# Optimization experiments

Measured on AMD Instinct MI355X. Metric: run time of the kernel, lower is better.

## Reference

```python
import jax, jax.numpy as jnp
import numpy as np

D_MODEL = 1024
N_HEADS = 16
D_KV = 64
B, S = 2, 2048


def setup_inputs() -> dict:
    key = jax.random.key(0)
    ks = jax.random.split(key, 7)
    scale = 1.0 / np.sqrt(D_MODEL)
    return {
        "query": jax.random.normal(ks[0], (B, S, D_MODEL), jnp.float32),
        "key": jax.random.normal(ks[1], (B, S, D_MODEL), jnp.float32),
        "value": jax.random.normal(ks[2], (B, S, D_MODEL), jnp.float32),
        "mask": jnp.zeros((B, 1, 1, S), jnp.float32),
        "Wq": jax.random.normal(ks[3], (D_MODEL, N_HEADS * D_KV), jnp.float32) * scale,
        "Wk": jax.random.normal(ks[4], (D_MODEL, N_HEADS * D_KV), jnp.float32) * scale,
        "Wv": jax.random.normal(ks[5], (D_MODEL, N_HEADS * D_KV), jnp.float32) * scale,
        "Wo": jax.random.normal(ks[6], (N_HEADS * D_KV, D_MODEL), jnp.float32) * scale,
    }


def _split_heads(x):
    b, s, _ = x.shape
    return x.reshape(b, s, N_HEADS, D_KV).transpose(0, 2, 1, 3)  # [B,H,S,Dk]


def reference(query, key, value, mask, Wq, Wk, Wv, Wo):
    q = _split_heads(query @ Wq)
    k = _split_heads(key @ Wk)
    v = _split_heads(value @ Wv)
    scores = jnp.einsum("bhqd,bhkd->bhqk", q, k) / jnp.sqrt(
        jnp.asarray(D_KV, scores_dtype := q.dtype)
    )
    scores = scores + mask
    attn = jax.nn.softmax(scores, axis=-1)  # dropout_rate=0 -> identity
    ctx = jnp.einsum("bhqk,bhkd->bhqd", attn, v)
    ctx = ctx.transpose(0, 2, 1, 3).reshape(query.shape[0], -1, N_HEADS * D_KV)
    hidden = ctx @ Wo
    return hidden
```

## Files before the change

kernel.cpp:

```cpp
#include <hip/hip_runtime.h>
#include <hip/hip_bf16.h>
#include <stdint.h>

typedef __bf16 bf16;
typedef __bf16 bf16x8 __attribute__((ext_vector_type(8)));
typedef __bf16 bf16x4 __attribute__((ext_vector_type(4)));
typedef float  f32x4  __attribute__((ext_vector_type(4)));
typedef float  f32x16 __attribute__((ext_vector_type(16)));

#define S_LEN  2048
#define NH     16
#define DKV    64
#define DMODEL 1024
#define LOG2E  1.4426950408889634f

__device__ __forceinline__ void async_load16(const void* g, void* l) {
  __builtin_amdgcn_global_load_lds(
      (const __attribute__((address_space(1))) uint32_t*)(uintptr_t)g,
      (__attribute__((address_space(3))) uint32_t*)(uintptr_t)l,
      16, 0, 0);
}

__global__ void cast_qkv(const float* __restrict__ q, const float* __restrict__ k,
                         const float* __restrict__ v,
                         bf16* __restrict__ qo, bf16* __restrict__ ko, bf16* __restrict__ vo)
{
  int z = blockIdx.y;
  const float* in = (z == 0) ? q : (z == 1) ? k : v;
  bf16* out = (z == 0) ? qo : (z == 1) ? ko : vo;
  int i = blockIdx.x * 256 + threadIdx.x;
  const float4* in4 = (const float4*)in;
  float4 a = in4[2 * i];
  float4 c = in4[2 * i + 1];
  bf16x8 o;
  o[0] = (bf16)a.x; o[1] = (bf16)a.y; o[2] = (bf16)a.z; o[3] = (bf16)a.w;
  o[4] = (bf16)c.x; o[5] = (bf16)c.y; o[6] = (bf16)c.z; o[7] = (bf16)c.w;
  ((bf16x8*)out)[i] = o;
}

__global__ void transpose_w(const float* __restrict__ W0, const float* __restrict__ W1,
                            const float* __restrict__ W2, const float* __restrict__ W3,
                            bf16* __restrict__ T0, bf16* __restrict__ T1,
                            bf16* __restrict__ T2, bf16* __restrict__ T3)
{
  int z = blockIdx.z;
  const float* W = (z == 0) ? W0 : (z == 1) ? W1 : (z == 2) ? W2 : W3;
  bf16* T = (z == 0) ? T0 : (z == 1) ? T1 : (z == 2) ? T2 : T3;
  __shared__ float tile[32][33];
  int n0 = blockIdx.x * 32, k0 = blockIdx.y * 32;
  int tx = threadIdx.x, ty = threadIdx.y;
  for (int i = 0; i < 32; i += 8)
    tile[ty + i][tx] = W[(size_t)(k0 + ty + i) * DMODEL + n0 + tx];
  __syncthreads();
  for (int i = 0; i < 32; i += 8)
    T[(size_t)(n0 + ty + i) * DMODEL + k0 + tx] = (bf16)tile[tx][ty + i];
}

template<int TM, int MODE>
__global__ __launch_bounds__(256) void gemm_bt(
    const bf16* __restrict__ A0, const bf16* __restrict__ A1, const bf16* __restrict__ A2,
    const bf16* __restrict__ B0, const bf16* __restrict__ B1, const bf16* __restrict__ B2,
    void* __restrict__ C0, void* __restrict__ C1, void* __restrict__ C2,
    int M, int N, int K)
{
  constexpr int MI = TM / 32;
  __shared__ __align__(16) bf16 As[TM * 32];
  __shared__ __align__(16) bf16 Bs[128 * 32];
  int z = blockIdx.z;
  const bf16* A  = (z == 0) ? A0 : (z == 1) ? A1 : A2;
  const bf16* Bt = (z == 0) ? B0 : (z == 1) ? B1 : B2;
  void* C        = (z == 0) ? C0 : (z == 1) ? C1 : C2;

  const int m0 = blockIdx.y * TM;
  const int n0 = blockIdx.x * 128;
  const int tid = threadIdx.x;
  const int lane = tid & 63;
  const int wave = tid >> 6;
  const int wm = (wave >> 1) * (TM / 2);
  const int wn = (wave & 1) * 64;
  const int row = lane & 15;
  const int quad = lane >> 4;

  f32x4 acc[MI][4];
  for (int i = 0; i < MI; ++i)
    for (int j = 0; j < 4; ++j) acc[i][j] = (f32x4){0.f, 0.f, 0.f, 0.f};

  const int nk = K >> 5;
  for (int kt = 0; kt < nk; ++kt) {
    __syncthreads();
    const int kk = kt << 5;
    for (int j = 0; j < TM / 64; ++j) {
      int base = j * 256 + wave * 64;
      int idx = base + lane;
      int r = idx >> 2;
      int cb = (idx & 3) << 4;
      async_load16((const char*)(A + (size_t)(m0 + r) * K + kk) + cb,
                   (char*)As + (size_t)base * 16);
    }
    for (int j = 0; j < 2; ++j) {
      int base = j * 256 + wave * 64;
      int idx = base + lane;
      int r = idx >> 2;
      int cb = (idx & 3) << 4;
      async_load16((const char*)(Bt + (size_t)(n0 + r) * K + kk) + cb,
                   (char*)Bs + (size_t)base * 16);
    }
    __syncthreads();
    bf16x8 af[MI], bfr[4];
    for (int i = 0; i < MI; ++i)
      af[i] = *(const bf16x8*)(As + (wm + i * 16 + row) * 32 + quad * 8);
    for (int j = 0; j < 4; ++j)
      bfr[j] = *(const bf16x8*)(Bs + (wn + j * 16 + row) * 32 + quad * 8);
    for (int i = 0; i < MI; ++i)
      for (int j = 0; j < 4; ++j)
        acc[i][j] = __builtin_amdgcn_mfma_f32_16x16x32_bf16(af[i], bfr[j], acc[i][j], 0, 0, 0);
  }

  if (MODE == 0) {
    float* Cf = (float*)C;
    for (int i = 0; i < MI; ++i)
      for (int j = 0; j < 4; ++j)
        for (int r = 0; r < 4; ++r) {
          int gm = m0 + wm + i * 16 + quad * 4 + r;
          int gn = n0 + wn + j * 16 + row;
          Cf[(size_t)gm * N + gn] = acc[i][j][r];
        }
  } else if (z != 2) {
    bf16* Cb = (bf16*)C;
    for (int i = 0; i < MI; ++i)
      for (int j = 0; j < 4; ++j)
        for (int r = 0; r < 4; ++r) {
          int gm = m0 + wm + i * 16 + quad * 4 + r;
          int gn = n0 + wn + j * 16 + row;
          int b = gm >> 11, s = gm & 2047;
          int h = gn >> 6,  d = gn & 63;
          Cb[(((size_t)(b * NH + h)) * S_LEN + s) * DKV + d] = (bf16)acc[i][j][r];
        }
  } else {
    bf16* Cb = (bf16*)C;
    for (int i = 0; i < MI; ++i)
      for (int j = 0; j < 4; ++j) {
        int gm = m0 + wm + i * 16 + quad * 4;
        int gn = n0 + wn + j * 16 + row;
        int b = gm >> 11, s = gm & 2047;
        int h = gn >> 6,  d = gn & 63;
        bf16x4 t;
        for (int r = 0; r < 4; ++r) t[r] = (bf16)acc[i][j][r];
        *(bf16x4*)(Cb + (((size_t)(b * NH + h)) * DKV + d) * S_LEN + s) = t;
      }
  }
}

__global__ __launch_bounds__(256, 4) void attn_kernel(
    const bf16* __restrict__ Qh, const bf16* __restrict__ Kh, const bf16* __restrict__ Vth,
    const float* __restrict__ mask, bf16* __restrict__ ctx)
{
  __shared__ __align__(16) bf16 Ks[64 * 64];
  __shared__ __align__(16) bf16 Kext[64 * 16];
  __shared__ __align__(16) bf16 Vts[64 * 64];
  __shared__ __align__(16) float lsumS[4 * 32];

  const int bh = blockIdx.y;
  const int b = bh >> 4;
  const int h = bh & 15;
  const int q0 = blockIdx.x * 128;
  const int tid = threadIdx.x;
  const int lane = tid & 63;
  const int wave = tid >> 6;
  const int ln = lane & 31;
  const int hi = lane >> 5;
  const float SC2 = 0.125f * LOG2E;

  const int qg = q0 + wave * 32 + ln;
  bf16x8 qf[5];
  {
    const bf16* qrow = Qh + ((size_t)bh * S_LEN + qg) * DKV;
    for (int c = 0; c < 4; ++c)
      qf[c] = *(const bf16x8*)(qrow + c * 16 + hi * 8);
    bf16x8 z;
    for (int u = 0; u < 8; ++u) z[u] = (bf16)0.f;
    if (hi == 0) z[0] = (bf16)1.0f;
    qf[4] = z;
  }

  f32x16 O[2];
  for (int nb = 0; nb < 2; ++nb)
    for (int i = 0; i < 16; ++i) O[nb][i] = 0.f;
  float lsum = 0.f;

  for (int kv0 = 0; kv0 < S_LEN; kv0 += 64) {
    __syncthreads();
    for (int j = 0; j < 2; ++j) {
      int base = j * 256 + wave * 64;
      int idx = base + lane;
      int r = idx >> 3;
      int cc = (idx & 7) ^ (r & 7);
      async_load16(Kh + ((size_t)bh * S_LEN + kv0 + r) * DKV + cc * 8,
                   (char*)Ks + (size_t)base * 16);
      async_load16(Vth + ((size_t)bh * DKV + r) * S_LEN + kv0 + cc * 8,
                   (char*)Vts + (size_t)base * 16);
    }
    if (tid < 64) {
      float m8 = mask[b * S_LEN + kv0 + tid] * 8.0f;
      bf16x8 e0, zz;
      for (int u = 0; u < 8; ++u) { e0[u] = (bf16)0.f; zz[u] = (bf16)0.f; }
      e0[0] = (bf16)m8;
      *(bf16x8*)(Kext + tid * 16)     = e0;
      *(bf16x8*)(Kext + tid * 16 + 8) = zz;
    }
    __syncthreads();

    f32x16 Sm[2];
    for (int i = 0; i < 16; ++i) { Sm[0][i] = 0.f; Sm[1][i] = 0.f; }
    for (int c = 0; c < 5; ++c) {
      bf16x8 k0, k1;
      if (c < 4) {
        k0 = *(const bf16x8*)(Ks + (ln)      * 64 + (((2 * c + hi) ^ (ln & 7)) << 3));
        k1 = *(const bf16x8*)(Ks + (32 + ln) * 64 + (((2 * c + hi) ^ (ln & 7)) << 3));
      } else {
        k0 = *(const bf16x8*)(Kext + ln * 16 + hi * 8);
        k1 = *(const bf16x8*)(Kext + (32 + ln) * 16 + hi * 8);
      }
      Sm[0] = __builtin_amdgcn_mfma_f32_32x32x16_bf16(k0, qf[c], Sm[0], 0, 0, 0);
      Sm[1] = __builtin_amdgcn_mfma_f32_32x32x16_bf16(k1, qf[c], Sm[1], 0, 0, 0);
    }

    for (int cg = 0; cg < 4; ++cg) {
      int mb = cg >> 1, g = cg & 1;
      bf16x8 ap;
      float ls0 = 0.f;
      for (int u = 0; u < 8; ++u) {
        float p = __builtin_amdgcn_exp2f(Sm[mb][g * 8 + u] * SC2);
        ls0 += p;
        ap[u] = (bf16)p;
      }
      lsum += ls0;
      for (int nb = 0; nb < 2; ++nb) {
        int d = nb * 32 + ln;
        int ch0 = ((2 * g + 4 * mb))     ^ (d & 7);
        int ch1 = ((1 + 2 * g + 4 * mb)) ^ (d & 7);
        bf16x4 lo = *(const bf16x4*)(Vts + d * 64 + ch0 * 8 + hi * 4);
        bf16x4 hv = *(const bf16x4*)(Vts + d * 64 + ch1 * 8 + hi * 4);
        bf16x8 bv;
        for (int u = 0; u < 4; ++u) { bv[u] = lo[u]; bv[u + 4] = hv[u]; }
        O[nb] = __builtin_amdgcn_mfma_f32_32x32x16_bf16(ap, bv, O[nb], 0, 0, 0);
      }
    }
  }

  float lt = lsum + __shfl_xor(lsum, 32, 64);
  if (lane < 32) lsumS[wave * 32 + lane] = 1.0f / lt;
  __builtin_amdgcn_s_waitcnt(0);

  for (int g = 0; g < 4; ++g) {
    f32x4 ri = *(const f32x4*)(lsumS + wave * 32 + g * 8 + hi * 4);
    for (int nb = 0; nb < 2; ++nb)
      for (int j = 0; j < 4; ++j) {
        int qrow = q0 + wave * 32 + j + 8 * g + 4 * hi;
        float v = O[nb][g * 4 + j] * ri[j];
        ctx[((size_t)b * S_LEN + qrow) * DMODEL + h * DKV + nb * 32 + ln] = (bf16)v;
      }
  }
}

extern "C" void kernel_launch(void* const* d_in, const int* in_sizes, int n_in,
                              void* d_out, int out_size, void* d_ws, size_t ws_size,
                              hipStream_t stream)
{
  const float* query = (const float*)d_in[0];
  const float* key_  = (const float*)d_in[1];
  const float* value = (const float*)d_in[2];
  const float* mask  = (const float*)d_in[3];
  const float* Wq = (const float*)d_in[4];
  const float* Wk = (const float*)d_in[5];
  const float* Wv = (const float*)d_in[6];
  const float* Wo = (const float*)d_in[7];

  char* ws = (char*)d_ws;
  const size_t MB = (size_t)1 << 20;
  bf16* qb  = (bf16*)(ws + 0 * MB);
  bf16* kb  = (bf16*)(ws + 8 * MB);
  bf16* vb  = (bf16*)(ws + 16 * MB);
  bf16* wqt = (bf16*)(ws + 24 * MB);
  bf16* wkt = (bf16*)(ws + 26 * MB);
  bf16* wvt = (bf16*)(ws + 28 * MB);
  bf16* wot = (bf16*)(ws + 30 * MB);
  bf16* qh  = (bf16*)(ws + 32 * MB);
  bf16* kh  = (bf16*)(ws + 40 * MB);
  bf16* vth = (bf16*)(ws + 48 * MB);
  bf16* ctx = (bf16*)(ws + 0 * MB);

  cast_qkv<<<dim3(2048, 3), 256, 0, stream>>>(query, key_, value, qb, kb, vb);
  transpose_w<<<dim3(32, 32, 4), dim3(32, 8), 0, stream>>>(Wq, Wk, Wv, Wo, wqt, wkt, wvt, wot);
  gemm_bt<128, 1><<<dim3(8, 32, 3), 256, 0, stream>>>(qb, kb, vb, wqt, wkt, wvt,
                                                      (void*)qh, (void*)kh, (void*)vth,
                                                      4096, 1024, 1024);
  attn_kernel<<<dim3(16, 32), 256, 0, stream>>>(qh, kh, vth, mask, ctx);
  gemm_bt<64, 0><<<dim3(8, 64, 1), 256, 0, stream>>>(ctx, ctx, ctx, wot, wot, wot,
                                                     d_out, d_out, d_out,
                                                     4096, 1024, 1024);
}
```

Baseline: 251.5 us.

## Split attention over two KV halves, add combine kernel, pre-permute V tiles

The attention kernel now splits the key/value sequence into two halves along a new grid dimension, writing unnormalized fp32 partial outputs and row sums, and a new combine kernel sums them, normalizes and writes bf16 context. The V projection epilogue writes V in a tile-permuted layout, so each 64x64 tile loads contiguously and reads no longer need XOR swizzle. The mask is added in fp32 before exp2 instead of through an extra MFMA step. This doubles the attention grid to fill more CUs, at the cost of an extra launch and fp32 partial-result traffic. Softmax still skips max subtraction, so the split needs no rescaling.

```diff
diff --git a/kernel.cpp b/kernel.cpp
--- a/kernel.cpp
+++ b/kernel.cpp
@@ -144,26 +144,27 @@
         int gn = n0 + wn + j * 16 + row;
         int b = gm >> 11, s = gm & 2047;
         int h = gn >> 6,  d = gn & 63;
+        int bh = b * NH + h;
+        int tile = s >> 6, kb = (s & 63) >> 2;
         bf16x4 t;
         for (int r = 0; r < 4; ++r) t[r] = (bf16)acc[i][j][r];
-        *(bf16x4*)(Cb + (((size_t)(b * NH + h)) * DKV + d) * S_LEN + s) = t;
+        *(bf16x4*)(Cb + ((((size_t)bh * 32 + tile) * 16 + kb) * 64 + d) * 4) = t;
       }
   }
 }
 
 __global__ __launch_bounds__(256, 4) void attn_kernel(
-    const bf16* __restrict__ Qh, const bf16* __restrict__ Kh, const bf16* __restrict__ Vth,
-    const float* __restrict__ mask, bf16* __restrict__ ctx)
+    const bf16* __restrict__ Qh, const bf16* __restrict__ Kh, const bf16* __restrict__ Vperm,
+    const float* __restrict__ mask, float* __restrict__ Opart, float* __restrict__ Lpart)
 {
   __shared__ __align__(16) bf16 Ks[64 * 64];
-  __shared__ __align__(16) bf16 Kext[64 * 16];
   __shared__ __align__(16) bf16 Vts[64 * 64];
-  __shared__ __align__(16) float lsumS[4 * 32];
+  __shared__ __align__(16) float masks2[64];
 
   const int bh = blockIdx.y;
   const int b = bh >> 4;
-  const int h = bh & 15;
   const int q0 = blockIdx.x * 128;
+  const int zh = blockIdx.z;
   const int tid = threadIdx.x;
   const int lane = tid & 63;
   const int wave = tid >> 6;
@@ -172,15 +173,11 @@
   const float SC2 = 0.125f * LOG2E;
 
   const int qg = q0 + wave * 32 + ln;
-  bf16x8 qf[5];
+  bf16x8 qf[4];
   {
     const bf16* qrow = Qh + ((size_t)bh * S_LEN + qg) * DKV;
     for (int c = 0; c < 4; ++c)
       qf[c] = *(const bf16x8*)(qrow + c * 16 + hi * 8);
-    bf16x8 z;
-    for (int u = 0; u < 8; ++u) z[u] = (bf16)0.f;
-    if (hi == 0) z[0] = (bf16)1.0f;
-    qf[4] = z;
   }
 
   f32x16 O[2];
@@ -188,8 +185,10 @@
     for (int i = 0; i < 16; ++i) O[nb][i] = 0.f;
   float lsum = 0.f;
 
-  for (int kv0 = 0; kv0 < S_LEN; kv0 += 64) {
+  for (int it = 0; it < 16; ++it) {
+    const int kv0 = zh * 1024 + it * 64;
     __syncthreads();
+    const bf16* vtile = Vperm + ((size_t)bh * 32 + (kv0 >> 6)) * (64 * 64);
     for (int j = 0; j < 2; ++j) {
       int base = j * 256 + wave * 64;
       int idx = base + lane;
@@ -197,50 +196,42 @@
       int cc = (idx & 7) ^ (r & 7);
       async_load16(Kh + ((size_t)bh * S_LEN + kv0 + r) * DKV + cc * 8,
                    (char*)Ks + (size_t)base * 16);
-      async_load16(Vth + ((size_t)bh * DKV + r) * S_LEN + kv0 + cc * 8,
+      async_load16(vtile + (size_t)idx * 8,
                    (char*)Vts + (size_t)base * 16);
     }
-    if (tid < 64) {
-      float m8 = mask[b * S_LEN + kv0 + tid] * 8.0f;
-      bf16x8 e0, zz;
-      for (int u = 0; u < 8; ++u) { e0[u] = (bf16)0.f; zz[u] = (bf16)0.f; }
-      e0[0] = (bf16)m8;
-      *(bf16x8*)(Kext + tid * 16)     = e0;
-      *(bf16x8*)(Kext + tid * 16 + 8) = zz;
-    }
+    if (tid < 64) masks2[tid] = mask[b * S_LEN + kv0 + tid] * LOG2E;
     __syncthreads();
 
     f32x16 Sm[2];
     for (int i = 0; i < 16; ++i) { Sm[0][i] = 0.f; Sm[1][i] = 0.f; }
-    for (int c = 0; c < 5; ++c) {
-      bf16x8 k0, k1;
-      if (c < 4) {
-        k0 = *(const bf16x8*)(Ks + (ln)      * 64 + (((2 * c + hi) ^ (ln & 7)) << 3));
-        k1 = *(const bf16x8*)(Ks + (32 + ln) * 64 + (((2 * c + hi) ^ (ln & 7)) << 3));
-      } else {
-        k0 = *(const bf16x8*)(Kext + ln * 16 + hi * 8);
-        k1 = *(const bf16x8*)(Kext + (32 + ln) * 16 + hi * 8);
-      }
+    for (int c = 0; c < 4; ++c) {
+      bf16x8 k0 = *(const bf16x8*)(Ks + ln * 64        + (((2 * c + hi) ^ (ln & 7)) << 3));
+      bf16x8 k1 = *(const bf16x8*)(Ks + (32 + ln) * 64 + (((2 * c + hi) ^ (ln & 7)) << 3));
       Sm[0] = __builtin_amdgcn_mfma_f32_32x32x16_bf16(k0, qf[c], Sm[0], 0, 0, 0);
       Sm[1] = __builtin_amdgcn_mfma_f32_32x32x16_bf16(k1, qf[c], Sm[1], 0, 0, 0);
     }
 
     for (int cg = 0; cg < 4; ++cg) {
       int mb = cg >> 1, g = cg & 1;
+      int koff = 32 * mb + 16 * g + 4 * hi;
+      f32x4 mklo = *(const f32x4*)(masks2 + koff);
+      f32x4 mkhi = *(const f32x4*)(masks2 + koff + 8);
       bf16x8 ap;
       float ls0 = 0.f;
-      for (int u = 0; u < 8; ++u) {
-        float p = __builtin_amdgcn_exp2f(Sm[mb][g * 8 + u] * SC2);
-        ls0 += p;
-        ap[u] = (bf16)p;
+      for (int u = 0; u < 4; ++u) {
+        float p = __builtin_amdgcn_exp2f(Sm[mb][g * 8 + u] * SC2 + mklo[u]);
+        ls0 += p; ap[u] = (bf16)p;
+      }
+      for (int u = 0; u < 4; ++u) {
+        float p = __builtin_amdgcn_exp2f(Sm[mb][g * 8 + 4 + u] * SC2 + mkhi[u]);
+        ls0 += p; ap[4 + u] = (bf16)p;
       }
       lsum += ls0;
+      int kb0 = hi + 4 * g + 8 * mb;
       for (int nb = 0; nb < 2; ++nb) {
         int d = nb * 32 + ln;
-        int ch0 = ((2 * g + 4 * mb))     ^ (d & 7);
-        int ch1 = ((1 + 2 * g + 4 * mb)) ^ (d & 7);
-        bf16x4 lo = *(const bf16x4*)(Vts + d * 64 + ch0 * 8 + hi * 4);
-        bf16x4 hv = *(const bf16x4*)(Vts + d * 64 + ch1 * 8 + hi * 4);
+        bf16x4 lo = *(const bf16x4*)(Vts + ((size_t)kb0 * 64 + d) * 4);
+        bf16x4 hv = *(const bf16x4*)(Vts + ((size_t)(kb0 + 2) * 64 + d) * 4);
         bf16x8 bv;
         for (int u = 0; u < 4; ++u) { bv[u] = lo[u]; bv[u + 4] = hv[u]; }
         O[nb] = __builtin_amdgcn_mfma_f32_32x32x16_bf16(ap, bv, O[nb], 0, 0, 0);
@@ -249,18 +240,36 @@
   }
 
   float lt = lsum + __shfl_xor(lsum, 32, 64);
-  if (lane < 32) lsumS[wave * 32 + lane] = 1.0f / lt;
-  __builtin_amdgcn_s_waitcnt(0);
-
-  for (int g = 0; g < 4; ++g) {
-    f32x4 ri = *(const f32x4*)(lsumS + wave * 32 + g * 8 + hi * 4);
+  if (lane < 32)
+    Lpart[((size_t)zh * 32 + bh) * S_LEN + q0 + wave * 32 + ln] = lt;
+
+  float* ob = Opart + (((size_t)zh * 32 + bh) * S_LEN) * DKV;
+  for (int g = 0; g < 4; ++g)
     for (int nb = 0; nb < 2; ++nb)
       for (int j = 0; j < 4; ++j) {
         int qrow = q0 + wave * 32 + j + 8 * g + 4 * hi;
-        float v = O[nb][g * 4 + j] * ri[j];
-        ctx[((size_t)b * S_LEN + qrow) * DMODEL + h * DKV + nb * 32 + ln] = (bf16)v;
-      }
-  }
+        ob[(size_t)qrow * DKV + nb * 32 + ln] = O[nb][g * 4 + j];
+      }
+}
+
+__global__ void combine_kernel(const float* __restrict__ Opart,
+                               const float* __restrict__ Lpart,
+                               bf16* __restrict__ ctx)
+{
+  int t = blockIdx.x * 256 + threadIdx.x;
+  int dg = t & 15;
+  int q  = (t >> 4) & 2047;
+  int bh = t >> 15;
+  int b = bh >> 4, h = bh & 15;
+  size_t o0 = ((size_t)bh * S_LEN + q) * DKV + dg * 4;
+  size_t o1 = ((size_t)(32 + bh) * S_LEN + q) * DKV + dg * 4;
+  f32x4 a = *(const f32x4*)(Opart + o0);
+  f32x4 c = *(const f32x4*)(Opart + o1);
+  float l = Lpart[(size_t)bh * S_LEN + q] + Lpart[(size_t)(32 + bh) * S_LEN + q];
+  float r = 1.0f / l;
+  bf16x4 o;
+  for (int u = 0; u < 4; ++u) o[u] = (bf16)((a[u] + c[u]) * r);
+  *(bf16x4*)(ctx + ((size_t)(b * S_LEN + q)) * DMODEL + h * DKV + dg * 4) = o;
 }
 
 extern "C" void kernel_launch(void* const* d_in, const int* in_sizes, int n_in,
@@ -278,24 +287,27 @@
 
   char* ws = (char*)d_ws;
   const size_t MB = (size_t)1 << 20;
-  bf16* qb  = (bf16*)(ws + 0 * MB);
-  bf16* kb  = (bf16*)(ws + 8 * MB);
-  bf16* vb  = (bf16*)(ws + 16 * MB);
-  bf16* wqt = (bf16*)(ws + 24 * MB);
-  bf16* wkt = (bf16*)(ws + 26 * MB);
-  bf16* wvt = (bf16*)(ws + 28 * MB);
-  bf16* wot = (bf16*)(ws + 30 * MB);
-  bf16* qh  = (bf16*)(ws + 32 * MB);
-  bf16* kh  = (bf16*)(ws + 40 * MB);
-  bf16* vth = (bf16*)(ws + 48 * MB);
-  bf16* ctx = (bf16*)(ws + 0 * MB);
+  bf16* qb    = (bf16*)(ws + 0 * MB);
+  bf16* kb    = (bf16*)(ws + 8 * MB);
+  bf16* vb    = (bf16*)(ws + 16 * MB);
+  bf16* wqt   = (bf16*)(ws + 24 * MB);
+  bf16* wkt   = (bf16*)(ws + 26 * MB);
+  bf16* wvt   = (bf16*)(ws + 28 * MB);
+  bf16* qh    = (bf16*)(ws + 32 * MB);
+  bf16* kh    = (bf16*)(ws + 40 * MB);
+  bf16* vperm = (bf16*)(ws + 48 * MB);
+  bf16* wot   = (bf16*)(ws + 56 * MB);
+  float* Opart = (float*)(ws + 0 * MB);
+  float* Lpart = (float*)(ws + 58 * MB);
+  bf16* ctx   = (bf16*)(ws + 32 * MB);
 
   cast_qkv<<<dim3(2048, 3), 256, 0, stream>>>(query, key_, value, qb, kb, vb);
   transpose_w<<<dim3(32, 32, 4), dim3(32, 8), 0, stream>>>(Wq, Wk, Wv, Wo, wqt, wkt, wvt, wot);
   gemm_bt<128, 1><<<dim3(8, 32, 3), 256, 0, stream>>>(qb, kb, vb, wqt, wkt, wvt,
-                                                      (void*)qh, (void*)kh, (void*)vth,
+                                                      (void*)qh, (void*)kh, (void*)vperm,
                                                       4096, 1024, 1024);
-  attn_kernel<<<dim3(16, 32), 256, 0, stream>>>(qh, kh, vth, mask, ctx);
+  attn_kernel<<<dim3(16, 32, 2), 256, 0, stream>>>(qh, kh, vperm, mask, Opart, Lpart);
+  combine_kernel<<<dim3(4096), 256, 0, stream>>>(Opart, Lpart, ctx);
   gemm_bt<64, 0><<<dim3(8, 64, 1), 256, 0, stream>>>(ctx, ctx, ctx, wot, wot, wot,
                                                      d_out, d_out, d_out,
                                                      4096, 1024, 1024);
```

New measurement: 231.4 us. 8.0% less time.
